# Kernel optimization log

Hardware: AMD Instinct MI355X
Metric: run time of the kernel (lower is better)

The kernel has to match this reference:

```python
import jax, jax.numpy as jnp
import numpy as np

NEG_SLOPE = 0.2

def _l2norm(x):
    # F.normalize(x, 2, -1): x / max(||x||_2, 1e-12)
    return x / jnp.maximum(jnp.linalg.norm(x, axis=-1, keepdims=True), 1e-12)

def _segment_softmax(e, dst, n_dst):
    m = jax.ops.segment_max(e, dst, num_segments=n_dst)
    m = jnp.where(jnp.isfinite(m), m, 0.0)
    ex = jnp.exp(e - m[dst])
    denom = jax.ops.segment_sum(ex, dst, num_segments=n_dst)
    return ex / (denom[dst] + 1e-16)

def _gat_conv(x_src, x_dst, edge_index, W, a_src, a_dst, b, n_dst):
    # PyG GATConv, heads=1, concat, shared lin for src/dst (int in_channels)
    h_src = x_src @ W                      # [Ns, H]
    h_dst = x_dst @ W                      # [Nd, H]
    src, dst = edge_index[0], edge_index[1]
    al_s = h_src @ a_src                   # [Ns]
    al_d = h_dst @ a_dst                   # [Nd]
    e = jax.nn.leaky_relu(al_s[src] + al_d[dst], NEG_SLOPE)  # [E]
    coef = _segment_softmax(e, dst, n_dst)                   # [E]
    out = jax.ops.segment_sum(coef[:, None] * h_src[src], dst, num_segments=n_dst)
    return out + b

def setup_inputs() -> dict:
    key = jax.random.key(0)
    ks = jax.random.split(key, 32)
    nd, npr, nc, H, L, B = 2000, 19000, 100, 256, 2, 8192
    E_pp, E_dp, E_cp = 400000, 60000, 300000
    s = 0.1
    inp = {
        'drug_emb': jax.random.normal(ks[0], (nd, H), jnp.float32),
        'protein_emb': jax.random.normal(ks[1], (npr, H), jnp.float32),
        'cell_emb': jax.random.normal(ks[2], (nc, H), jnp.float32),
        'W_pp': jax.random.normal(ks[3], (L, H, H), jnp.float32) * s,
        'as_pp': jax.random.normal(ks[4], (L, H), jnp.float32) * s,
        'ad_pp': jax.random.normal(ks[5], (L, H), jnp.float32) * s,
        'b_pp': jax.random.normal(ks[6], (L, H), jnp.float32) * s,
        'W_dp': jax.random.normal(ks[7], (L, H, H), jnp.float32) * s,
        'as_dp': jax.random.normal(ks[8], (L, H), jnp.float32) * s,
        'ad_dp': jax.random.normal(ks[9], (L, H), jnp.float32) * s,
        'b_dp': jax.random.normal(ks[10], (L, H), jnp.float32) * s,
        'W_cp': jax.random.normal(ks[11], (L, H, H), jnp.float32) * s,
        'as_cp': jax.random.normal(ks[12], (L, H), jnp.float32) * s,
        'ad_cp': jax.random.normal(ks[13], (L, H), jnp.float32) * s,
        'b_cp': jax.random.normal(ks[14], (L, H), jnp.float32) * s,
        'W1': jax.random.normal(ks[15], (3 * H, 6 * H), jnp.float32) * s,
        'b1': jax.random.normal(ks[16], (6 * H,), jnp.float32) * s,
        'W2': jax.random.normal(ks[17], (6 * H, 2 * H), jnp.float32) * s,
        'b2': jax.random.normal(ks[18], (2 * H,), jnp.float32) * s,
        'W3': jax.random.normal(ks[19], (2 * H, 2), jnp.float32) * s,
        'b3': jax.random.normal(ks[20], (2,), jnp.float32) * s,
        'edge_pp': jnp.stack([jax.random.randint(ks[21], (E_pp,), 0, npr),
                              jax.random.randint(ks[22], (E_pp,), 0, npr)]),
        'edge_dp': jnp.stack([jax.random.randint(ks[23], (E_dp,), 0, npr),
                              jax.random.randint(ks[24], (E_dp,), 0, nd)]),
        'edge_cp': jnp.stack([jax.random.randint(ks[25], (E_cp,), 0, npr),
                              jax.random.randint(ks[26], (E_cp,), 0, nc)]),
        'drug1': jax.random.randint(ks[27], (B,), 0, nd),
        'drug2': jax.random.randint(ks[28], (B,), 0, nd),
        'cell': jax.random.randint(ks[29], (B,), 0, nc),
    }
    return inp

def reference(drug_emb, protein_emb, cell_emb,
              W_pp, as_pp, ad_pp, b_pp,
              W_dp, as_dp, ad_dp, b_dp,
              W_cp, as_cp, ad_cp, b_cp,
              W1, b1, W2, b2, W3, b3,
              edge_pp, edge_dp, edge_cp, drug1, drug2, cell):
    n_drug, n_prot, n_cell = drug_emb.shape[0], protein_emb.shape[0], cell_emb.shape[0]
    num_layer = W_pp.shape[0]
    # node ids are arange -> embedding lookup is the full table
    x_d, x_p, x_c = drug_emb, protein_emb, cell_emb
    # p-p GATConv adds self loops (default add_self_loops=True)
    loop = jnp.arange(n_prot, dtype=edge_pp.dtype)
    ei_pp = jnp.concatenate([edge_pp, jnp.stack([loop, loop])], axis=1)
    for l in range(num_layer):
        x_p = _gat_conv(x_p, x_p, ei_pp, W_pp[l], as_pp[l], ad_pp[l], b_pp[l], n_prot)
        x_p = _l2norm(x_p)
        x_d = jax.nn.relu(_gat_conv(x_p, x_d, edge_dp, W_dp[l], as_dp[l], ad_dp[l], b_dp[l], n_drug))
        x_c = jax.nn.relu(_gat_conv(x_p, x_c, edge_cp, W_cp[l], as_cp[l], ad_cp[l], b_cp[l], n_cell))
    hid = jnp.concatenate([_l2norm(x_d[drug1]), _l2norm(x_d[drug2]), _l2norm(x_c[cell])], axis=1)
    h = jax.nn.relu(hid @ W1 + b1)
    h = jax.nn.relu(h @ W2 + b2)
    logits = h @ W3 + b3
    return logits
```

## Files before the change

### kernel.cpp

```cpp
#include <hip/hip_runtime.h>
#include <hip/hip_bf16.h>

#define HDIM 256
#define NEG_SLOPE 0.2f
#define NB 128
#define SLICES 8
#define TBN 64
#define TBK 32
#define PITCH 40

typedef __attribute__((ext_vector_type(8))) short bf16x8;
typedef __attribute__((ext_vector_type(4))) float f32x4;

__device__ inline uint f2pl(float x) {
  __hip_bfloat16 h = __float2bfloat16(x);
  ushort hi = *(ushort*)&h;
  float r = x - __bfloat162float(h);
  __hip_bfloat16 l = __float2bfloat16(r);
  ushort lo = *(ushort*)&l;
  return (uint)hi | ((uint)lo << 16);
}
__device__ inline ushort f2b(float x) {
  __hip_bfloat16 h = __float2bfloat16(x);
  return *(ushort*)&h;
}
__device__ inline float b2f(ushort u) {
  uint x = ((uint)u) << 16;
  return __int_as_float((int)x);
}

static inline int cdiv(int a, int b) { return (a + b - 1) / b; }

__global__ void fillf_kernel(float* __restrict__ p, float v, int n) {
  int i = blockIdx.x * blockDim.x + threadIdx.x;
  if (i < n) p[i] = v;
}

__global__ void wconv_split_kernel(const float* __restrict__ W,
                                   ushort* __restrict__ WTh, ushort* __restrict__ WTl,
                                   int K, int N) {
  int i = blockIdx.x * 256 + threadIdx.x;
  if (i >= K * N) return;
  int k = i / N, n = i - k * N;
  uint p = f2pl(W[i]);
  WTh[(size_t)n * K + k] = (ushort)(p & 0xffff);
  WTl[(size_t)n * K + k] = (ushort)(p >> 16);
}

__global__ void wconv_split3_kernel(
    const float* __restrict__ Wpp, const float* __restrict__ Wdp, const float* __restrict__ Wcp,
    ushort* __restrict__ WTpph, ushort* __restrict__ WTppl,
    ushort* __restrict__ WTdph, ushort* __restrict__ WTdpl,
    ushort* __restrict__ WTcph, ushort* __restrict__ WTcpl, int L) {
  const int per = HDIM * HDIM;
  int i = blockIdx.x * 256 + threadIdx.x;
  if (i >= 3 * L * per) return;
  int mat = i / per;
  int r = i - mat * per;
  int l = mat / 3, ty = mat - l * 3;
  const float* W = (ty == 0 ? Wpp : ty == 1 ? Wdp : Wcp) + (size_t)l * per;
  ushort* Th = (ty == 0 ? WTpph : ty == 1 ? WTdph : WTcph) + (size_t)l * per;
  ushort* Tl = (ty == 0 ? WTppl : ty == 1 ? WTdpl : WTcpl) + (size_t)l * per;
  int k = r >> 8, n = r & (HDIM - 1);
  uint p = f2pl(W[r]);
  Th[(size_t)n * HDIM + k] = (ushort)(p & 0xffff);
  Tl[(size_t)n * HDIM + k] = (ushort)(p >> 16);
}

__global__ void f32_to_b16_kernel(const float* __restrict__ in, ushort* __restrict__ out, int n) {
  int i = blockIdx.x * 256 + threadIdx.x;
  if (i < n) out[i] = f2b(in[i]);
}

__global__ void f32_to_split_kernel(const float* __restrict__ in,
                                    ushort* __restrict__ oh, ushort* __restrict__ ol, int n) {
  int i = blockIdx.x * 256 + threadIdx.x;
  if (i >= n) return;
  uint p = f2pl(in[i]);
  oh[i] = (ushort)(p & 0xffff);
  ol[i] = (ushort)(p >> 16);
}

__global__ __launch_bounds__(256) void matvec_all_kernel(
    const float* __restrict__ Wpp, const float* __restrict__ aspp, const float* __restrict__ adpp,
    const float* __restrict__ Wdp, const float* __restrict__ asdp, const float* __restrict__ addp,
    const float* __restrict__ Wcp, const float* __restrict__ ascp, const float* __restrict__ adcp,
    float* __restrict__ wv) {
  int b = blockIdx.x;
  int l = b / 6, r = b - l * 6, type = r >> 1, isd = r & 1;
  const float* W = (type == 0 ? Wpp : type == 1 ? Wdp : Wcp) + (size_t)l * HDIM * HDIM;
  const float* a = (type == 0 ? (isd ? adpp : aspp)
                  : type == 1 ? (isd ? addp : asdp)
                              : (isd ? adcp : ascp)) + (size_t)l * HDIM;
  int k = threadIdx.x;
  const float4* Wr = (const float4*)(W + (size_t)k * HDIM);
  float s = 0.f;
#pragma unroll 8
  for (int n4 = 0; n4 < HDIM / 4; ++n4) {
    float4 w = Wr[n4];
    float4 av = *(const float4*)(a + n4 * 4);
    s += w.x * av.x + w.y * av.y + w.z * av.z + w.w * av.w;
  }
  wv[(size_t)b * HDIM + k] = s;
}

__global__ __launch_bounds__(256) void combine_h1_kernel(
    const float* __restrict__ P1, const float* __restrict__ P2, const float* __restrict__ P3,
    const int* __restrict__ g1, const int* __restrict__ g2, const int* __restrict__ g3,
    int row0, ushort* __restrict__ h1h, ushort* __restrict__ h1l, int M, int K) {
  int t = blockIdx.x * 256 + threadIdx.x;
  int kq = K >> 2;
  if (t >= M * kq) return;
  int row = t / kq, c4 = t - row * kq;
  int bi = row0 + row;
  size_t o = (size_t)c4 * 4;
  float4 a = *(const float4*)(P1 + (size_t)g1[bi] * K + o);
  float4 b = *(const float4*)(P2 + (size_t)g2[bi] * K + o);
  float4 c = *(const float4*)(P3 + (size_t)g3[bi] * K + o);
  uint p0 = f2pl(fmaxf(a.x + b.x + c.x, 0.f));
  uint p1 = f2pl(fmaxf(a.y + b.y + c.y, 0.f));
  uint p2 = f2pl(fmaxf(a.z + b.z + c.z, 0.f));
  uint p3 = f2pl(fmaxf(a.w + b.w + c.w, 0.f));
  ushort4 h = {(ushort)(p0 & 0xffff), (ushort)(p1 & 0xffff), (ushort)(p2 & 0xffff), (ushort)(p3 & 0xffff)};
  ushort4 l = {(ushort)(p0 >> 16), (ushort)(p1 >> 16), (ushort)(p2 >> 16), (ushort)(p3 >> 16)};
  *(ushort4*)(h1h + (size_t)row * K + o) = h;
  *(ushort4*)(h1l + (size_t)row * K + o) = l;
}

template <int TBM_, int ACT>
__global__ __launch_bounds__(256) void mfma_gemm(
    const ushort* __restrict__ Ahg, const ushort* __restrict__ Alg,
    const ushort* __restrict__ Bhg, const ushort* __restrict__ Blg,
    int ldb, const float* __restrict__ bias,
    float* __restrict__ C, int M, int N, int K) {
  __shared__ __align__(16) ushort Ah[2][TBM_][PITCH];
  __shared__ __align__(16) ushort Al[2][TBM_][PITCH];
  __shared__ __align__(16) ushort Bh[2][TBN][PITCH];
  __shared__ __align__(16) ushort Bl[2][TBN][PITCH];

  constexpr int NU = TBM_ / 64;
  constexpr int TM = TBM_ / 32;

  const int tid = threadIdx.x;
  const int lane = tid & 63;
  const int wid = tid >> 6;
  const int wm = wid & 1, wn = wid >> 1;
  const int l16 = lane & 15;
  const int quad = lane >> 4;
  const int m0 = blockIdx.x * TBM_;
  const int n0 = blockIdx.y * TBN;

  const int co = (lane & 3) * 8;
  const int r4 = lane >> 2;

  uint4 rah0[NU], ral0[NU], rbh0, rbl0;
  uint4 rah1[NU], ral1[NU], rbh1, rbl1;

  auto LOADA = [&](uint4* rah, uint4* ral, uint4& rbh, uint4& rbl, int k0) {
#pragma unroll
    for (int u = 0; u < NU; ++u) {
      int r = wid * (TBM_ / 4) + r4 + 16 * u;
      int gm = m0 + r;
      if (gm < M) {
        size_t o = (size_t)gm * K + k0 + co;
        rah[u] = *(const uint4*)(Ahg + o);
        ral[u] = *(const uint4*)(Alg + o);
      } else {
        rah[u] = make_uint4(0, 0, 0, 0);
        ral[u] = make_uint4(0, 0, 0, 0);
      }
    }
    {
      int r = wid * 16 + r4;
      size_t o = (size_t)(n0 + r) * ldb + k0 + co;
      rbh = *(const uint4*)(Bhg + o);
      rbl = *(const uint4*)(Blg + o);
    }
  };
  auto STORE = [&](const uint4* rah, const uint4* ral, const uint4& rbh, const uint4& rbl, int b) {
#pragma unroll
    for (int u = 0; u < NU; ++u) {
      int r = wid * (TBM_ / 4) + r4 + 16 * u;
      *(uint4*)&Ah[b][r][co] = rah[u];
      *(uint4*)&Al[b][r][co] = ral[u];
    }
    int r = wid * 16 + r4;
    *(uint4*)&Bh[b][r][co] = rbh;
    *(uint4*)&Bl[b][r][co] = rbl;
  };

  f32x4 acc[TM][2];
#pragma unroll
  for (int i = 0; i < TM; ++i)
#pragma unroll
    for (int j = 0; j < 2; ++j) acc[i][j] = (f32x4){0.f, 0.f, 0.f, 0.f};

  auto COMPUTE = [&](int b) {
    bf16x8 ahf[TM], alf[TM], bhf[2], blf[2];
#pragma unroll
    for (int t = 0; t < TM; ++t) {
      int r = wm * (TBM_ / 2) + t * 16 + l16;
      ahf[t] = *(const bf16x8*)&Ah[b][r][quad * 8];
      alf[t] = *(const bf16x8*)&Al[b][r][quad * 8];
    }
#pragma unroll
    for (int t = 0; t < 2; ++t) {
      int r = wn * 32 + t * 16 + l16;
      bhf[t] = *(const bf16x8*)&Bh[b][r][quad * 8];
      blf[t] = *(const bf16x8*)&Bl[b][r][quad * 8];
    }
#pragma unroll
    for (int tm = 0; tm < TM; ++tm)
#pragma unroll
      for (int tn = 0; tn < 2; ++tn) {
        acc[tm][tn] = __builtin_amdgcn_mfma_f32_16x16x32_bf16(ahf[tm], bhf[tn], acc[tm][tn], 0, 0, 0);
        acc[tm][tn] = __builtin_amdgcn_mfma_f32_16x16x32_bf16(ahf[tm], blf[tn], acc[tm][tn], 0, 0, 0);
        acc[tm][tn] = __builtin_amdgcn_mfma_f32_16x16x32_bf16(alf[tm], bhf[tn], acc[tm][tn], 0, 0, 0);
      }
  };

  const int NK = K / TBK;
  LOADA(rah0, ral0, rbh0, rbl0, 0);
  LOADA(rah1, ral1, rbh1, rbl1, TBK);
  STORE(rah0, ral0, rbh0, rbl0, 0);
  int k = 2 * TBK;
  for (int t = 0; t < (NK - 2) / 2; ++t) {
    __syncthreads();
    LOADA(rah0, ral0, rbh0, rbl0, k);
    COMPUTE(0);
    STORE(rah1, ral1, rbh1, rbl1, 1);
    k += TBK;
    __syncthreads();
    LOADA(rah1, ral1, rbh1, rbl1, k);
    COMPUTE(1);
    STORE(rah0, ral0, rbh0, rbl0, 0);
    k += TBK;
  }
  __syncthreads();
  COMPUTE(0);
  STORE(rah1, ral1, rbh1, rbl1, 1);
  __syncthreads();
  COMPUTE(1);

#pragma unroll
  for (int tn = 0; tn < 2; ++tn) {
    int col = n0 + wn * 32 + tn * 16 + l16;
    float bv = bias ? bias[col] : 0.f;
#pragma unroll
    for (int tm = 0; tm < TM; ++tm) {
#pragma unroll
      for (int r = 0; r < 4; ++r) {
        int row = m0 + wm * (TBM_ / 2) + tm * 16 + quad * 4 + r;
        if (row >= M) continue;
        float v = acc[tm][tn][r] + bv;
        if (ACT == 1) v = fmaxf(v, 0.f);
        C[(size_t)row * N + col] = v;
      }
    }
  }
}

template <int TBM_, int ACT>
static void gemm_launch(hipStream_t s,
                        const ushort* Ahg, const ushort* Alg,
                        const ushort* Bhg, const ushort* Blg,
                        int ldb, const float* bias, float* C,
                        int M, int N, int K) {
  dim3 g(cdiv(M, TBM_), N / TBN);
  mfma_gemm<TBM_, ACT><<<g, 256, 0, s>>>(Ahg, Alg, Bhg, Blg, ldb, bias, C, M, N, K);
}

__global__ __launch_bounds__(256) void rowdot_kernel(
    const float* __restrict__ H, const float* __restrict__ a,
    float* __restrict__ out, int n) {
  int row = blockIdx.x * 4 + (threadIdx.x >> 6);
  if (row >= n) return;
  int lane = threadIdx.x & 63;
  const float* h = H + (size_t)row * HDIM;
  float s = 0.f;
#pragma unroll
  for (int u = 0; u < 4; ++u) {
    int c = lane + u * 64;
    s += h[c] * a[c];
  }
#pragma unroll
  for (int off = 32; off; off >>= 1) s += __shfl_down(s, off);
  if (lane == 0) out[row] = s;
}

__global__ __launch_bounds__(256) void rowdot2_kernel(
    const float* __restrict__ H, const float* __restrict__ a1, const float* __restrict__ a2,
    float* __restrict__ o1, float* __restrict__ o2, int n) {
  int row = blockIdx.x * 4 + (threadIdx.x >> 6);
  if (row >= n) return;
  int lane = threadIdx.x & 63;
  const float* h = H + (size_t)row * HDIM;
  float s1 = 0.f, s2 = 0.f;
#pragma unroll
  for (int u = 0; u < 4; ++u) {
    int c = lane + u * 64;
    float hv = h[c];
    s1 += hv * a1[c];
    s2 += hv * a2[c];
  }
#pragma unroll
  for (int off = 32; off; off >>= 1) {
    s1 += __shfl_down(s1, off);
    s2 += __shfl_down(s2, off);
  }
  if (lane == 0) { o1[row] = s1; o2[row] = s2; }
}

__global__ __launch_bounds__(256) void hist_kernel(
    const int* __restrict__ src, const int* __restrict__ dst, int E, int nloops,
    int Nd, int* __restrict__ offs) {
  extern __shared__ int bins[];
  int tot = E + nloops;
  int chunk = (tot + NB - 1) / NB;
  int b = blockIdx.x;
  int s0 = b * chunk, s1 = min(s0 + chunk, tot);
  for (int i = threadIdx.x; i < Nd; i += 256) bins[i] = 0;
  __syncthreads();
  for (int i = s0 + threadIdx.x; i < s1; i += 256) {
    int d = (i < E) ? dst[i] : (i - E);
    atomicAdd(&bins[d], 1);
  }
  __syncthreads();
  for (int i = threadIdx.x; i < Nd; i += 256) offs[(size_t)i * NB + b] = bins[i];
}

__global__ __launch_bounds__(256) void scan_bins_kernel(
    int* __restrict__ offs, int* __restrict__ binsum, int Nd) {
  int d = blockIdx.x * 4 + (threadIdx.x >> 6);
  if (d >= Nd) return;
  int lane = threadIdx.x & 63;
  int* p = offs + (size_t)d * NB;
  int v0 = p[2 * lane], v1 = p[2 * lane + 1];
  int s = v0 + v1;
  int t = s;
#pragma unroll
  for (int o = 1; o < 64; o <<= 1) { int u = __shfl_up(t, o); if (lane >= o) t += u; }
  int excl = t - s;
  p[2 * lane] = excl;
  p[2 * lane + 1] = excl + v0;
  if (lane == 63) binsum[d] = t;
}

__global__ __launch_bounds__(256) void scan_base_kernel(
    const int* __restrict__ binsum, int* __restrict__ rowptr, int Nd) {
  __shared__ int wsum[4];
  __shared__ int carry;
  if (threadIdx.x == 0) carry = 0;
  __syncthreads();
  int lane = threadIdx.x & 63, w = threadIdx.x >> 6;
  for (int t0 = 0; t0 < Nd; t0 += 256) {
    int i = t0 + threadIdx.x;
    int v = (i < Nd) ? binsum[i] : 0;
    int t = v;
#pragma unroll
    for (int o = 1; o < 64; o <<= 1) { int u = __shfl_up(t, o); if (lane >= o) t += u; }
    if (lane == 63) wsum[w] = t;
    __syncthreads();
    int add = carry;
    for (int k = 0; k < w; ++k) add += wsum[k];
    if (i < Nd) rowptr[i] = t - v + add;
    __syncthreads();
    if (threadIdx.x == 0) carry += wsum[0] + wsum[1] + wsum[2] + wsum[3];
    __syncthreads();
  }
  if (threadIdx.x == 0) rowptr[Nd] = carry;
}

__global__ __launch_bounds__(256) void scatter_kernel(
    const int* __restrict__ src, const int* __restrict__ dst, int E, int nloops,
    int Nd, const int* __restrict__ offs, const int* __restrict__ rowptr,
    uint* __restrict__ sd) {
  extern __shared__ int bins[];
  int tot = E + nloops;
  int chunk = (tot + NB - 1) / NB;
  int b = blockIdx.x;
  int s0 = b * chunk, s1 = min(s0 + chunk, tot);
  for (int i = threadIdx.x; i < Nd; i += 256) bins[i] = 0;
  __syncthreads();
  for (int i = s0 + threadIdx.x; i < s1; i += 256) {
    int s_, d_;
    if (i < E) { s_ = src[i]; d_ = dst[i]; }
    else       { s_ = d_ = i - E; }
    int local = atomicAdd(&bins[d_], 1);
    int pos = rowptr[d_] + offs[(size_t)d_ * NB + b] + local;
    sd[pos] = (uint)s_ | ((uint)d_ << 16);
  }
}

__global__ __launch_bounds__(256) void gat_agg_split(
    const int* __restrict__ rowptr, const uint* __restrict__ sd,
    const float* __restrict__ als, const float* __restrict__ ald,
    const ushort* __restrict__ Xb,
    ushort* __restrict__ aggh, ushort* __restrict__ aggl, int n) {
  int d = blockIdx.x * 4 + (threadIdx.x >> 6);
  if (d >= n) return;
  int lane = threadIdx.x & 63;
  int r0 = rowptr[d], r1 = rowptr[d + 1];
  float aldd = ald[d];
  float dsum = 0.f;
  for (int j = r0 + lane; j < r1; j += 64) {
    float e = als[sd[j] & 0xffff] + aldd;
    e = (e > 0.f) ? e : NEG_SLOPE * e;
    dsum += __expf(e);
  }
#pragma unroll
  for (int o = 32; o; o >>= 1) dsum += __shfl_xor(dsum, o);
  float rden = 1.f / (dsum + 1e-16f);

  float4 acc = make_float4(0.f, 0.f, 0.f, 0.f);
  for (int b = r0; b < r1; b += 64) {
    int j = b + lane;
    float exv = 0.f; int srcv = 0;
    if (j < r1) {
      uint p = sd[j];
      srcv = p & 0xffff;
      float e = als[srcv] + aldd;
      e = (e > 0.f) ? e : NEG_SLOPE * e;
      exv = __expf(e) * rden;
    }
    int cnt = min(64, r1 - b);
    for (int t0 = 0; t0 < cnt; t0 += 8) {
      float cf[8]; int sv[8];
#pragma unroll
      for (int u = 0; u < 8; ++u) {
        cf[u] = __shfl(exv, t0 + u);
        sv[u] = __shfl(srcv, t0 + u);
      }
      ushort4 hv[8];
#pragma unroll
      for (int u = 0; u < 8; ++u)
        hv[u] = *(const ushort4*)(Xb + (size_t)sv[u] * HDIM + lane * 4);
#pragma unroll
      for (int u = 0; u < 8; ++u) {
        acc.x += cf[u] * b2f(hv[u].x);
        acc.y += cf[u] * b2f(hv[u].y);
        acc.z += cf[u] * b2f(hv[u].z);
        acc.w += cf[u] * b2f(hv[u].w);
      }
    }
  }
  uint p0 = f2pl(acc.x), p1 = f2pl(acc.y), p2 = f2pl(acc.z), p3 = f2pl(acc.w);
  ushort4 h = {(ushort)(p0 & 0xffff), (ushort)(p1 & 0xffff), (ushort)(p2 & 0xffff), (ushort)(p3 & 0xffff)};
  ushort4 l = {(ushort)(p0 >> 16), (ushort)(p1 >> 16), (ushort)(p2 >> 16), (ushort)(p3 >> 16)};
  *(ushort4*)(aggh + (size_t)d * HDIM + lane * 4) = h;
  *(ushort4*)(aggl + (size_t)d * HDIM + lane * 4) = l;
}

__global__ __launch_bounds__(256) void gat_agg_slice(
    const int* __restrict__ rowptr, const uint* __restrict__ sd,
    const float* __restrict__ als, const float* __restrict__ ald,
    const ushort* __restrict__ Xb, float* __restrict__ out32, int n) {
  int d = blockIdx.x / SLICES;
  int sl = blockIdx.x - d * SLICES;
  if (d >= n) return;
  int lane = threadIdx.x & 63, w = threadIdx.x >> 6;
  int r0 = rowptr[d], r1 = rowptr[d + 1];
  float aldd = ald[d];
  float dsum = 0.f;
  for (int j = r0 + threadIdx.x; j < r1; j += 256) {
    float e = als[sd[j] & 0xffff] + aldd;
    e = (e > 0.f) ? e : NEG_SLOPE * e;
    dsum += __expf(e);
  }
#pragma unroll
  for (int o = 32; o; o >>= 1) dsum += __shfl_xor(dsum, o);
  __shared__ float wd[4];
  if (lane == 0) wd[w] = dsum;
  __syncthreads();
  float rden = 1.f / (wd[0] + wd[1] + wd[2] + wd[3] + 1e-16f);
  int deg = r1 - r0;
  int per_b = (deg + SLICES - 1) / SLICES;
  int b0 = r0 + sl * per_b, b1 = min(b0 + per_b, r1);
  int wdeg = b1 - b0;
  if (wdeg <= 0) return;
  int per_w = (wdeg + 3) >> 2;
  int w0 = b0 + w * per_w, w1 = min(w0 + per_w, b1);

  float4 acc = make_float4(0.f, 0.f, 0.f, 0.f);
  for (int b = w0; b < w1; b += 64) {
    int j = b + lane;
    float exv = 0.f; int srcv = 0;
    if (j < w1) {
      uint p = sd[j];
      srcv = p & 0xffff;
      float e = als[srcv] + aldd;
      e = (e > 0.f) ? e : NEG_SLOPE * e;
      exv = __expf(e) * rden;
    }
    int cnt = min(64, w1 - b);
    for (int t0 = 0; t0 < cnt; t0 += 8) {
      float cf[8]; int sv[8];
#pragma unroll
      for (int u = 0; u < 8; ++u) {
        cf[u] = __shfl(exv, t0 + u);
        sv[u] = __shfl(srcv, t0 + u);
      }
      ushort4 hv[8];
#pragma unroll
      for (int u = 0; u < 8; ++u)
        hv[u] = *(const ushort4*)(Xb + (size_t)sv[u] * HDIM + lane * 4);
#pragma unroll
      for (int u = 0; u < 8; ++u) {
        acc.x += cf[u] * b2f(hv[u].x);
        acc.y += cf[u] * b2f(hv[u].y);
        acc.z += cf[u] * b2f(hv[u].z);
        acc.w += cf[u] * b2f(hv[u].w);
      }
    }
  }
  float* o = out32 + (size_t)d * HDIM + lane * 4;
  atomicAdd(o + 0, acc.x); atomicAdd(o + 1, acc.y);
  atomicAdd(o + 2, acc.z); atomicAdd(o + 3, acc.w);
}

__global__ __launch_bounds__(256) void l2norm_f32b_dots_kernel(
    const float* __restrict__ in, float* __restrict__ outf, ushort* __restrict__ outb,
    const float* __restrict__ v1, const float* __restrict__ v2,
    const float* __restrict__ v3, const float* __restrict__ v4,
    float* __restrict__ o1, float* __restrict__ o2,
    float* __restrict__ o3, float* __restrict__ o4, int n) {
  int row = blockIdx.x * 4 + (threadIdx.x >> 6);
  if (row >= n) return;
  int lane = threadIdx.x & 63;
  float v[4];
  float ss = 0.f;
#pragma unroll
  for (int u = 0; u < 4; ++u) {
    float t = in[(size_t)row * HDIM + lane + u * 64];
    v[u] = t; ss += t * t;
  }
#pragma unroll
  for (int off = 32; off; off >>= 1) ss += __shfl_xor(ss, off);
  float sc = 1.0f / fmaxf(sqrtf(ss), 1e-12f);
  float d1 = 0.f, d2 = 0.f, d3 = 0.f, d4 = 0.f;
#pragma unroll
  for (int u = 0; u < 4; ++u) {
    float f = v[u] * sc;
    int c = lane + u * 64;
    outf[(size_t)row * HDIM + c] = f;
    outb[(size_t)row * HDIM + c] = f2b(f);
    d1 += f * v1[c];
    d2 += f * v2[c];
    if (o3) { d3 += f * v3[c]; d4 += f * v4[c]; }
  }
#pragma unroll
  for (int off = 32; off; off >>= 1) {
    d1 += __shfl_xor(d1, off);
    d2 += __shfl_xor(d2, off);
    if (o3) { d3 += __shfl_xor(d3, off); d4 += __shfl_xor(d4, off); }
  }
  if (lane == 0) {
    o1[row] = d1; o2[row] = d2;
    if (o3) { o3[row] = d3; o4[row] = d4; }
  }
}

__global__ __launch_bounds__(256) void l2norm_split_kernel(
    const float* __restrict__ in,
    ushort* __restrict__ oh, ushort* __restrict__ ol, int n) {
  int row = blockIdx.x * 4 + (threadIdx.x >> 6);
  if (row >= n) return;
  int lane = threadIdx.x & 63;
  float v[4];
  float ss = 0.f;
#pragma unroll
  for (int u = 0; u < 4; ++u) {
    int c = lane + u * 64;
    float t = in[(size_t)row * HDIM + c];
    v[u] = t;
    ss += t * t;
  }
#pragma unroll
  for (int off = 32; off; off >>= 1) ss += __shfl_xor(ss, off);
  float sc = 1.0f / fmaxf(sqrtf(ss), 1e-12f);
#pragma unroll
  for (int u = 0; u < 4; ++u) {
    int c = lane + u * 64;
    uint p = f2pl(v[u] * sc);
    oh[(size_t)row * HDIM + c] = (ushort)(p & 0xffff);
    ol[(size_t)row * HDIM + c] = (ushort)(p >> 16);
  }
}

__global__ __launch_bounds__(256) void head3_kernel(
    const float* __restrict__ h2, const float* __restrict__ W3, const float* __restrict__ b3,
    float* __restrict__ out, int M, int K) {
  int i = blockIdx.x * 4 + (threadIdx.x >> 6);
  int lane = threadIdx.x & 63;
  if (i >= M) return;
  float s0 = 0.f, s1 = 0.f;
  for (int k = lane; k < K; k += 64) {
    float h = h2[(size_t)i * K + k];
    s0 += h * W3[k * 2 + 0];
    s1 += h * W3[k * 2 + 1];
  }
#pragma unroll
  for (int off = 32; off; off >>= 1) {
    s0 += __shfl_down(s0, off);
    s1 += __shfl_down(s1, off);
  }
  if (lane == 0) {
    out[(size_t)i * 2 + 0] = s0 + b3[0];
    out[(size_t)i * 2 + 1] = s1 + b3[1];
  }
}

static void build_sorted(hipStream_t stream,
                         const int* src, const int* dst, int E, int nloops, int Nd,
                         int* offs, int* binsum, int* rowptr, uint* sd) {
  size_t lds = (size_t)Nd * sizeof(int);
  hist_kernel<<<NB, 256, lds, stream>>>(src, dst, E, nloops, Nd, offs);
  scan_bins_kernel<<<cdiv(Nd, 4), 256, 0, stream>>>(offs, binsum, Nd);
  scan_base_kernel<<<1, 256, 0, stream>>>(binsum, rowptr, Nd);
  scatter_kernel<<<NB, 256, lds, stream>>>(src, dst, E, nloops, Nd, offs, rowptr, sd);
}

extern "C" void kernel_launch(void* const* d_in, const int* in_sizes, int n_in,
                              void* d_out, int out_size, void* d_ws, size_t ws_size,
                              hipStream_t stream) {
  const float* drug_emb = (const float*)d_in[0];
  const float* prot_emb = (const float*)d_in[1];
  const float* cell_emb = (const float*)d_in[2];
  const float* W_pp = (const float*)d_in[3];
  const float* as_pp = (const float*)d_in[4];
  const float* ad_pp = (const float*)d_in[5];
  const float* b_pp = (const float*)d_in[6];
  const float* W_dp = (const float*)d_in[7];
  const float* as_dp = (const float*)d_in[8];
  const float* ad_dp = (const float*)d_in[9];
  const float* b_dp = (const float*)d_in[10];
  const float* W_cp = (const float*)d_in[11];
  const float* as_cp = (const float*)d_in[12];
  const float* ad_cp = (const float*)d_in[13];
  const float* b_cp = (const float*)d_in[14];
  const float* W1 = (const float*)d_in[15];
  const float* b1 = (const float*)d_in[16];
  const float* W2 = (const float*)d_in[17];
  const float* b2 = (const float*)d_in[18];
  const float* W3 = (const float*)d_in[19];
  const float* b3 = (const float*)d_in[20];
  const int* edge_pp = (const int*)d_in[21];
  const int* edge_dp = (const int*)d_in[22];
  const int* edge_cp = (const int*)d_in[23];
  const int* drug1 = (const int*)d_in[24];
  const int* drug2 = (const int*)d_in[25];
  const int* cellb = (const int*)d_in[26];

  const int ND = in_sizes[0] / HDIM;
  const int NP = in_sizes[1] / HDIM;
  const int NC = in_sizes[2] / HDIM;
  const int L = in_sizes[3] / (HDIM * HDIM);
  const int E_pp = in_sizes[21] / 2;
  const int E_dp = in_sizes[22] / 2;
  const int E_cp = in_sizes[23] / 2;
  const int B = in_sizes[24];
  (void)n_in; (void)out_size;

  const int* src_pp = edge_pp;          const int* dst_pp = edge_pp + E_pp;
  const int* src_dp = edge_dp;          const int* dst_dp = edge_dp + E_dp;
  const int* src_cp = edge_cp;          const int* dst_cp = edge_cp + E_cp;
  const int tot_pp = E_pp + NP, tot_dp = E_dp, tot_cp = E_cp;
  int maxN = NP > ND ? NP : ND; if (NC > maxN) maxN = NC;

  char* wsb = (char*)d_ws;
  size_t off = 0;
  auto alloc = [&](size_t bytes) -> void* {
    void* p = wsb + off;
    off += (bytes + 255) & ~(size_t)255;
    return p;
  };

  float* Xp  = (float*)alloc((size_t)NP * HDIM * 4);
  ushort* Xpb = (ushort*)alloc((size_t)NP * HDIM * 2);
  float* Xd  = (float*)alloc((size_t)ND * HDIM * 4);
  float* Xc  = (float*)alloc((size_t)NC * HDIM * 4);
  ushort* xdnh = (ushort*)alloc((size_t)ND * HDIM * 2);
  ushort* xdnl = (ushort*)alloc((size_t)ND * HDIM * 2);
  ushort* xcnh = (ushort*)alloc((size_t)NC * HDIM * 2);
  ushort* xcnl = (ushort*)alloc((size_t)NC * HDIM * 2);
  ushort* WTpph = (ushort*)alloc((size_t)L * HDIM * HDIM * 2);
  ushort* WTppl = (ushort*)alloc((size_t)L * HDIM * HDIM * 2);
  ushort* WTdph = (ushort*)alloc((size_t)L * HDIM * HDIM * 2);
  ushort* WTdpl = (ushort*)alloc((size_t)L * HDIM * HDIM * 2);
  ushort* WTcph = (ushort*)alloc((size_t)L * HDIM * HDIM * 2);
  ushort* WTcpl = (ushort*)alloc((size_t)L * HDIM * HDIM * 2);
  ushort* cth = (ushort*)alloc((size_t)NC * HDIM * 2);
  ushort* ctl = (ushort*)alloc((size_t)NC * HDIM * 2);
  float* wv  = (float*)alloc((size_t)L * 6 * HDIM * 4);
  float* pals = (float*)alloc((size_t)maxN * 4);
  float* pald = (float*)alloc((size_t)maxN * 4);
  float* als1 = (float*)alloc((size_t)maxN * 4);
  float* als2 = (float*)alloc((size_t)maxN * 4);
  float* ald1 = (float*)alloc((size_t)maxN * 4);
  float* ald2 = (float*)alloc((size_t)maxN * 4);
  int* binsum = (int*)alloc((size_t)maxN * 4);
  int* rp_pp = (int*)alloc((size_t)(NP + 1) * 4);
  int* rp_dp = (int*)alloc((size_t)(ND + 1) * 4);
  int* rp_cp = (int*)alloc((size_t)(NC + 1) * 4);
  uint* sd_pp = (uint*)alloc((size_t)tot_pp * 4);
  uint* sd_dp = (uint*)alloc((size_t)tot_dp * 4);
  uint* sd_cp = (uint*)alloc((size_t)tot_cp * 4);
  float* out32 = (float*)alloc((size_t)NC * HDIM * 4);
  size_t S0 = off;

  int* offs = (int*)(wsb + S0);
  build_sorted(stream, src_pp, dst_pp, E_pp, NP, NP, offs, binsum, rp_pp, sd_pp);
  build_sorted(stream, src_dp, dst_dp, E_dp, 0, ND, offs, binsum, rp_dp, sd_dp);
  build_sorted(stream, src_cp, dst_cp, E_cp, 0, NC, offs, binsum, rp_cp, sd_cp);

  wconv_split3_kernel<<<cdiv(3 * L * HDIM * HDIM, 256), 256, 0, stream>>>(
      W_pp, W_dp, W_cp, WTpph, WTppl, WTdph, WTdpl, WTcph, WTcpl, L);
  matvec_all_kernel<<<L * 6, 256, 0, stream>>>(W_pp, as_pp, ad_pp, W_dp, as_dp, ad_dp,
                                               W_cp, as_cp, ad_cp, wv);
  f32_to_b16_kernel<<<cdiv(NP * HDIM, 256), 256, 0, stream>>>(prot_emb, Xpb, NP * HDIM);

  size_t aggB = ((size_t)NP * HDIM * 2 + 255) & ~(size_t)255;
  ushort* aggh = (ushort*)(wsb + S0);
  ushort* aggl = (ushort*)(wsb + S0 + aggB);
  float* tmp = (float*)(wsb + S0 + 2 * aggB);

  rowdot2_kernel<<<cdiv(NP, 4), 256, 0, stream>>>(prot_emb, wv + 0 * HDIM, wv + 1 * HDIM,
                                                  pals, pald, NP);

  for (int l = 0; l < L; ++l) {
    const int WOFF = l * HDIM * HDIM, VOFF = l * HDIM;
    const float* wvl = wv + (size_t)l * 6 * HDIM;
    const float* wvn = wv + (size_t)(l + 1) * 6 * HDIM;
    const float* Xd_cur = (l == 0) ? drug_emb : Xd;
    const float* Xc_cur = (l == 0) ? cell_emb : Xc;
    bool last = (l == L - 1);

    gat_agg_split<<<cdiv(NP, 4), 256, 0, stream>>>(rp_pp, sd_pp, pals, pald, Xpb, aggh, aggl, NP);
    gemm_launch<128, 0>(stream, aggh, aggl, WTpph + WOFF, WTppl + WOFF, HDIM,
                        b_pp + VOFF, tmp, NP, HDIM, HDIM);
    l2norm_f32b_dots_kernel<<<cdiv(NP, 4), 256, 0, stream>>>(
        tmp, Xp, Xpb,
        wvl + 2 * HDIM, wvl + 4 * HDIM,
        last ? nullptr : (wvn + 0 * HDIM), last ? nullptr : (wvn + 1 * HDIM),
        als1, als2, last ? nullptr : pals, last ? nullptr : pald, NP);

    rowdot_kernel<<<cdiv(ND, 4), 256, 0, stream>>>(Xd_cur, wvl + 3 * HDIM, ald1, ND);
    rowdot_kernel<<<cdiv(NC, 4), 256, 0, stream>>>(Xc_cur, wvl + 5 * HDIM, ald2, NC);

    gat_agg_split<<<cdiv(ND, 4), 256, 0, stream>>>(rp_dp, sd_dp, als1, ald1, Xpb, aggh, aggl, ND);
    gemm_launch<64, 1>(stream, aggh, aggl, WTdph + WOFF, WTdpl + WOFF, HDIM,
                       b_dp + VOFF, Xd, ND, HDIM, HDIM);

    fillf_kernel<<<cdiv(NC * HDIM, 256), 256, 0, stream>>>(out32, 0.f, NC * HDIM);
    gat_agg_slice<<<NC * SLICES, 256, 0, stream>>>(rp_cp, sd_cp, als2, ald2, Xpb, out32, NC);
    f32_to_split_kernel<<<cdiv(NC * HDIM, 256), 256, 0, stream>>>(out32, cth, ctl, NC * HDIM);
    gemm_launch<64, 1>(stream, cth, ctl, WTcph + WOFF, WTcpl + WOFF, HDIM,
                       b_cp + VOFF, Xc, NC, HDIM, HDIM);
  }

  l2norm_split_kernel<<<cdiv(ND, 4), 256, 0, stream>>>(Xd, xdnh, xdnl, ND);
  l2norm_split_kernel<<<cdiv(NC, 4), 256, 0, stream>>>(Xc, xcnh, xcnl, NC);

  const int N1 = 6 * HDIM;
  const int N2 = 2 * HDIM;
  const int K1 = 3 * HDIM;
  ushort* W1Th = (ushort*)(wsb + S0);
  ushort* W1Tl = W1Th + (size_t)N1 * K1;
  ushort* W2Th = W1Tl + (size_t)N1 * K1;
  ushort* W2Tl = W2Th + (size_t)N2 * N1;
  float* P1 = (float*)(W2Tl + (size_t)N2 * N1);
  float* P2 = P1 + (size_t)ND * N1;
  float* P3 = P2 + (size_t)ND * N1;
  ushort* h1h = (ushort*)(P3 + (size_t)NC * N1);
  size_t wsz = ws_size ? ws_size : ((size_t)1 << 30);
  size_t fixed = S0 + ((size_t)N1 * K1 + (size_t)N2 * N1) * 4
               + ((size_t)(2 * ND + NC) * N1) * 4;
  int CH = 8192;
  while (CH > 1024 && fixed + (size_t)CH * (N1 * 4 + N2 * 4) > wsz) CH >>= 1;
  ushort* h1l = h1h + (size_t)CH * N1;
  float* h2 = (float*)(h1l + (size_t)CH * N1);

  wconv_split_kernel<<<cdiv(K1 * N1, 256), 256, 0, stream>>>(W1, W1Th, W1Tl, K1, N1);
  wconv_split_kernel<<<cdiv(N1 * N2, 256), 256, 0, stream>>>(W2, W2Th, W2Tl, N1, N2);

  gemm_launch<64, 0>(stream, xdnh, xdnl, W1Th, W1Tl, K1, nullptr, P1, ND, N1, HDIM);
  gemm_launch<64, 0>(stream, xdnh, xdnl, W1Th + HDIM, W1Tl + HDIM, K1, nullptr, P2, ND, N1, HDIM);
  gemm_launch<64, 0>(stream, xcnh, xcnl, W1Th + 2 * HDIM, W1Tl + 2 * HDIM, K1, b1, P3, NC, N1, HDIM);

  float* outp = (float*)d_out;
  for (int c0 = 0; c0 < B; c0 += CH) {
    int M = (B - c0) < CH ? (B - c0) : CH;
    combine_h1_kernel<<<cdiv(M * (N1 / 4), 256), 256, 0, stream>>>(
        P1, P2, P3, drug1, drug2, cellb, c0, h1h, h1l, M, N1);
    gemm_launch<128, 1>(stream, h1h, h1l, W2Th, W2Tl, N1, b2, h2, M, N2, N1);
    head3_kernel<<<cdiv(M, 4), 256, 0, stream>>>(h2, W3, b3, outp + (size_t)c0 * 2, M, N2);
  }
}
```

Baseline: 717.6 us.

## Fuse final head layer into MLP GEMM epilogue and reorganize LDS layout

The W2 GEMM epilogue now applies bias and ReLU, dots each row with W3, reduces across lanes, and atomically adds partial logits into an output pre-filled with b3. This removes the h2 intermediate buffer and the separate head3 kernel. The shared-memory tiles also move from padded rows to a k-group-major [4][rows][8] layout, meant to reduce bank conflicts. Atomics make the summation order nondeterministic, and each output element receives several atomic adds.

```diff
diff --git a/kernel.cpp b/kernel.cpp
--- a/kernel.cpp
+++ b/kernel.cpp
@@ -7,7 +7,6 @@
 #define SLICES 8
 #define TBN 64
 #define TBK 32
-#define PITCH 40
 
 typedef __attribute__((ext_vector_type(8))) short bf16x8;
 typedef __attribute__((ext_vector_type(4))) float f32x4;
@@ -34,6 +33,13 @@
 __global__ void fillf_kernel(float* __restrict__ p, float v, int n) {
   int i = blockIdx.x * blockDim.x + threadIdx.x;
   if (i < n) p[i] = v;
+}
+
+__global__ void fill_out2_kernel(float* __restrict__ out, const float* __restrict__ b3, int M) {
+  int i = blockIdx.x * 256 + threadIdx.x;
+  if (i >= M) return;
+  out[(size_t)i * 2 + 0] = b3[0];
+  out[(size_t)i * 2 + 1] = b3[1];
 }
 
 __global__ void wconv_split_kernel(const float* __restrict__ W,
@@ -127,16 +133,16 @@
   *(ushort4*)(h1l + (size_t)row * K + o) = l;
 }
 
-template <int TBM_, int ACT>
+template <int TBM_, int ACT, int FUSE3>
 __global__ __launch_bounds__(256) void mfma_gemm(
     const ushort* __restrict__ Ahg, const ushort* __restrict__ Alg,
     const ushort* __restrict__ Bhg, const ushort* __restrict__ Blg,
-    int ldb, const float* __restrict__ bias,
+    int ldb, const float* __restrict__ bias, const float* __restrict__ W3g,
     float* __restrict__ C, int M, int N, int K) {
-  __shared__ __align__(16) ushort Ah[2][TBM_][PITCH];
-  __shared__ __align__(16) ushort Al[2][TBM_][PITCH];
-  __shared__ __align__(16) ushort Bh[2][TBN][PITCH];
-  __shared__ __align__(16) ushort Bl[2][TBN][PITCH];
+  __shared__ __align__(16) ushort Ah[2][4][TBM_][8];
+  __shared__ __align__(16) ushort Al[2][4][TBM_][8];
+  __shared__ __align__(16) ushort Bh[2][4][TBN][8];
+  __shared__ __align__(16) ushort Bl[2][4][TBN][8];
 
   constexpr int NU = TBM_ / 64;
   constexpr int TM = TBM_ / 32;
@@ -150,7 +156,8 @@
   const int m0 = blockIdx.x * TBM_;
   const int n0 = blockIdx.y * TBN;
 
-  const int co = (lane & 3) * 8;
+  const int gq = lane & 3;
+  const int co = gq * 8;
   const int r4 = lane >> 2;
 
   uint4 rah0[NU], ral0[NU], rbh0, rbl0;
@@ -181,12 +188,12 @@
 #pragma unroll
     for (int u = 0; u < NU; ++u) {
       int r = wid * (TBM_ / 4) + r4 + 16 * u;
-      *(uint4*)&Ah[b][r][co] = rah[u];
-      *(uint4*)&Al[b][r][co] = ral[u];
+      *(uint4*)&Ah[b][gq][r][0] = rah[u];
+      *(uint4*)&Al[b][gq][r][0] = ral[u];
     }
     int r = wid * 16 + r4;
-    *(uint4*)&Bh[b][r][co] = rbh;
-    *(uint4*)&Bl[b][r][co] = rbl;
+    *(uint4*)&Bh[b][gq][r][0] = rbh;
+    *(uint4*)&Bl[b][gq][r][0] = rbl;
   };
 
   f32x4 acc[TM][2];
@@ -200,14 +207,14 @@
 #pragma unroll
     for (int t = 0; t < TM; ++t) {
       int r = wm * (TBM_ / 2) + t * 16 + l16;
-      ahf[t] = *(const bf16x8*)&Ah[b][r][quad * 8];
-      alf[t] = *(const bf16x8*)&Al[b][r][quad * 8];
+      ahf[t] = *(const bf16x8*)&Ah[b][quad][r][0];
+      alf[t] = *(const bf16x8*)&Al[b][quad][r][0];
     }
 #pragma unroll
     for (int t = 0; t < 2; ++t) {
       int r = wn * 32 + t * 16 + l16;
-      bhf[t] = *(const bf16x8*)&Bh[b][r][quad * 8];
-      blf[t] = *(const bf16x8*)&Bl[b][r][quad * 8];
+      bhf[t] = *(const bf16x8*)&Bh[b][quad][r][0];
+      blf[t] = *(const bf16x8*)&Bl[b][quad][r][0];
     }
 #pragma unroll
     for (int tm = 0; tm < TM; ++tm)
@@ -242,19 +249,46 @@
   __syncthreads();
   COMPUTE(1);
 
-#pragma unroll
-  for (int tn = 0; tn < 2; ++tn) {
-    int col = n0 + wn * 32 + tn * 16 + l16;
-    float bv = bias ? bias[col] : 0.f;
+  if (FUSE3) {
 #pragma unroll
     for (int tm = 0; tm < TM; ++tm) {
 #pragma unroll
       for (int r = 0; r < 4; ++r) {
         int row = m0 + wm * (TBM_ / 2) + tm * 16 + quad * 4 + r;
-        if (row >= M) continue;
-        float v = acc[tm][tn][r] + bv;
-        if (ACT == 1) v = fmaxf(v, 0.f);
-        C[(size_t)row * N + col] = v;
+        float s0 = 0.f, s1 = 0.f;
+#pragma unroll
+        for (int tn = 0; tn < 2; ++tn) {
+          int col = n0 + wn * 32 + tn * 16 + l16;
+          float v = fmaxf(acc[tm][tn][r] + bias[col], 0.f);
+          s0 += v * W3g[col * 2 + 0];
+          s1 += v * W3g[col * 2 + 1];
+        }
+#pragma unroll
+        for (int o = 1; o < 16; o <<= 1) {
+          s0 += __shfl_xor(s0, o);
+          s1 += __shfl_xor(s1, o);
+        }
+        if (l16 == 0 && row < M) {
+          atomicAdd(&C[(size_t)row * 2 + 0], s0);
+          atomicAdd(&C[(size_t)row * 2 + 1], s1);
+        }
+      }
+    }
+  } else {
+#pragma unroll
+    for (int tn = 0; tn < 2; ++tn) {
+      int col = n0 + wn * 32 + tn * 16 + l16;
+      float bv = bias ? bias[col] : 0.f;
+#pragma unroll
+      for (int tm = 0; tm < TM; ++tm) {
+#pragma unroll
+        for (int r = 0; r < 4; ++r) {
+          int row = m0 + wm * (TBM_ / 2) + tm * 16 + quad * 4 + r;
+          if (row >= M) continue;
+          float v = acc[tm][tn][r] + bv;
+          if (ACT == 1) v = fmaxf(v, 0.f);
+          C[(size_t)row * N + col] = v;
+        }
       }
     }
   }
@@ -267,7 +301,16 @@
                         int ldb, const float* bias, float* C,
                         int M, int N, int K) {
   dim3 g(cdiv(M, TBM_), N / TBN);
-  mfma_gemm<TBM_, ACT><<<g, 256, 0, s>>>(Ahg, Alg, Bhg, Blg, ldb, bias, C, M, N, K);
+  mfma_gemm<TBM_, ACT, 0><<<g, 256, 0, s>>>(Ahg, Alg, Bhg, Blg, ldb, bias, nullptr, C, M, N, K);
+}
+
+static void gemm_launch_f3(hipStream_t s,
+                           const ushort* Ahg, const ushort* Alg,
+                           const ushort* Bhg, const ushort* Blg,
+                           int ldb, const float* bias, const float* W3,
+                           float* C, int M, int N, int K) {
+  dim3 g(cdiv(M, 128), N / TBN);
+  mfma_gemm<128, 1, 1><<<g, 256, 0, s>>>(Ahg, Alg, Bhg, Blg, ldb, bias, W3, C, M, N, K);
 }
 
 __global__ __launch_bounds__(256) void rowdot_kernel(
@@ -584,29 +627,6 @@
     uint p = f2pl(v[u] * sc);
     oh[(size_t)row * HDIM + c] = (ushort)(p & 0xffff);
     ol[(size_t)row * HDIM + c] = (ushort)(p >> 16);
-  }
-}
-
-__global__ __launch_bounds__(256) void head3_kernel(
-    const float* __restrict__ h2, const float* __restrict__ W3, const float* __restrict__ b3,
-    float* __restrict__ out, int M, int K) {
-  int i = blockIdx.x * 4 + (threadIdx.x >> 6);
-  int lane = threadIdx.x & 63;
-  if (i >= M) return;
-  float s0 = 0.f, s1 = 0.f;
-  for (int k = lane; k < K; k += 64) {
-    float h = h2[(size_t)i * K + k];
-    s0 += h * W3[k * 2 + 0];
-    s1 += h * W3[k * 2 + 1];
-  }
-#pragma unroll
-  for (int off = 32; off; off >>= 1) {
-    s0 += __shfl_down(s0, off);
-    s1 += __shfl_down(s1, off);
-  }
-  if (lane == 0) {
-    out[(size_t)i * 2 + 0] = s0 + b3[0];
-    out[(size_t)i * 2 + 1] = s1 + b3[1];
   }
 }
 
@@ -776,9 +796,8 @@
   size_t fixed = S0 + ((size_t)N1 * K1 + (size_t)N2 * N1) * 4
                + ((size_t)(2 * ND + NC) * N1) * 4;
   int CH = 8192;
-  while (CH > 1024 && fixed + (size_t)CH * (N1 * 4 + N2 * 4) > wsz) CH >>= 1;
+  while (CH > 1024 && fixed + (size_t)CH * N1 * 4 > wsz) CH >>= 1;
   ushort* h1l = h1h + (size_t)CH * N1;
-  float* h2 = (float*)(h1l + (size_t)CH * N1);
 
   wconv_split_kernel<<<cdiv(K1 * N1, 256), 256, 0, stream>>>(W1, W1Th, W1Tl, K1, N1);
   wconv_split_kernel<<<cdiv(N1 * N2, 256), 256, 0, stream>>>(W2, W2Th, W2Tl, N1, N2);
@@ -788,11 +807,12 @@
   gemm_launch<64, 0>(stream, xcnh, xcnl, W1Th + 2 * HDIM, W1Tl + 2 * HDIM, K1, b1, P3, NC, N1, HDIM);
 
   float* outp = (float*)d_out;
+  fill_out2_kernel<<<cdiv(B, 256), 256, 0, stream>>>(outp, b3, B);
   for (int c0 = 0; c0 < B; c0 += CH) {
     int M = (B - c0) < CH ? (B - c0) : CH;
     combine_h1_kernel<<<cdiv(M * (N1 / 4), 256), 256, 0, stream>>>(
         P1, P2, P3, drug1, drug2, cellb, c0, h1h, h1l, M, N1);
-    gemm_launch<128, 1>(stream, h1h, h1l, W2Th, W2Tl, N1, b2, h2, M, N2, N1);
-    head3_kernel<<<cdiv(M, 4), 256, 0, stream>>>(h2, W3, b3, outp + (size_t)c0 * 2, M, N2);
-  }
-}
+    gemm_launch_f3(stream, h1h, h1l, W2Th, W2Tl, N1, b2, W3,
+                   outp + (size_t)c0 * 2, M, N2, N1);
+  }
+}
```

Result: no change. 714.9 us (-0.4%).
